# Optimization experiments

Measured on AMD Instinct MI355X. Metric: run time of the kernel, lower is better.

## Reference

```python
import jax, jax.numpy as jnp
import numpy as np

P = 22536   # priors
B = 32      # batch
M = 16      # objects per image (fixed for jit)
C = 81      # classes incl. background
THRESHOLD = 0.5
ALPHA_REG = 1.0   # config.reg_weights
FL_ALPHA = 0.25
FL_GAMMA = 2.0
EPS = 1e-7


def cxcy_to_xy(c):
    return jnp.concatenate([c[..., :2] - c[..., 2:] / 2, c[..., :2] + c[..., 2:] / 2], -1)


def gcxgcy_to_cxcy(g, p):
    return jnp.concatenate([g[..., :2] * p[..., 2:] / 10 + p[..., :2],
                            jnp.exp(g[..., 2:] / 5) * p[..., 2:]], -1)


def iou_xy(a, b):
    # a: (M,4) xyxy, b: (P,4) xyxy -> (M,P)
    lt = jnp.maximum(a[:, None, :2], b[None, :, :2])
    rb = jnp.minimum(a[:, None, 2:], b[None, :, 2:])
    inter = jnp.prod(jnp.clip(rb - lt, 0.0), -1)
    area_a = jnp.prod(a[:, 2:] - a[:, :2], -1)
    area_b = jnp.prod(b[:, 2:] - b[:, :2], -1)
    return inter / (area_a[:, None] + area_b[None, :] - inter)


def diou_loss(p, g):
    # elementwise DIoU loss, p/g: (..., 4) xyxy -> (...)
    lt = jnp.maximum(p[..., :2], g[..., :2])
    rb = jnp.minimum(p[..., 2:], g[..., 2:])
    inter = jnp.prod(jnp.clip(rb - lt, 0.0), -1)
    ap = jnp.prod(p[..., 2:] - p[..., :2], -1)
    ag = jnp.prod(g[..., 2:] - g[..., :2], -1)
    iou = inter / (ap + ag - inter + EPS)
    cp = (p[..., :2] + p[..., 2:]) / 2
    cg = (g[..., :2] + g[..., 2:]) / 2
    d2 = jnp.sum((cp - cg) ** 2, -1)
    elt = jnp.minimum(p[..., :2], g[..., :2])
    erb = jnp.maximum(p[..., 2:], g[..., 2:])
    c2 = jnp.sum((erb - elt) ** 2, -1) + EPS
    return 1.0 - iou + d2 / c2


def match_image(boxes_i, labels_i, priors_xy):
    # boxes_i: (M,4), labels_i: (M,), priors_xy: (P,4)
    overlap = iou_xy(boxes_i, priors_xy)                 # (M,P)
    ofp = overlap.max(0)                                  # overlap_for_each_prior (P,)
    obj = jnp.argmax(overlap, 0)                          # object_for_each_prior (P,)
    pfo = jnp.argmax(overlap, 1)                          # prior_for_each_object (M,)
    obj = obj.at[pfo].set(jnp.arange(M))
    ofp = ofp.at[pfo].set(1.0)
    lab = labels_i[obj]                                   # (P,)
    lab_neg = jnp.where(ofp < THRESHOLD - 0.1, -1, lab)
    lab = jnp.where(ofp < THRESHOLD, 0, lab)
    true_locs = boxes_i[obj]                              # (P,4)
    return lab, lab_neg, true_locs


def setup_inputs() -> dict:
    key = jax.random.key(0)
    k1, k2, k3, k4, k5, k6, k7 = jax.random.split(key, 7)
    pcxy = jax.random.uniform(k1, (P, 2), minval=0.05, maxval=0.95)
    pwh = jax.random.uniform(k2, (P, 2), minval=0.02, maxval=0.3)
    priors_cxcy = jnp.concatenate([pcxy, pwh], -1)
    ctr = jax.random.uniform(k3, (B, M, 2), minval=0.2, maxval=0.8)
    wh = jax.random.uniform(k4, (B, M, 2), minval=0.05, maxval=0.3)
    boxes = jnp.concatenate([ctr - wh / 2, ctr + wh / 2], -1)
    labels = jax.random.randint(k5, (B, M), 1, C).astype(jnp.int32)
    predicted_locs = jax.random.normal(k6, (B, P, 4), dtype=jnp.float32)
    predicted_scores = jax.random.normal(k7, (B, P, C), dtype=jnp.float32)
    return {"predicted_locs": predicted_locs, "predicted_scores": predicted_scores,
            "boxes": boxes, "labels": labels, "priors_cxcy": priors_cxcy}


def reference(predicted_locs, predicted_scores, boxes, labels, priors_cxcy):
    priors_xy = cxcy_to_xy(priors_cxcy)
    lab, lab_neg, true_locs = jax.vmap(match_image, in_axes=(0, 0, None))(boxes, labels, priors_xy)
    decoded = cxcy_to_xy(gcxgcy_to_cxcy(predicted_locs, priors_cxcy))   # (B,P,4)
    pos = lab > 0
    neg = lab_neg == -1
    # DIoU localization loss, mean over positive priors
    loc = diou_loss(decoded, true_locs)                                 # (B,P)
    npos = jnp.maximum(pos.sum(), 1)
    loc_loss = jnp.sum(loc * pos) / npos
    # focal classification loss over union of positive and hard-negative priors
    logp = jax.nn.log_softmax(predicted_scores, -1)                     # (B,P,C)
    lp_t = jnp.take_along_axis(logp, lab[..., None], -1)[..., 0]        # (B,P)
    pt = jnp.exp(lp_t)
    fl = FL_ALPHA * (1.0 - pt) ** FL_GAMMA * (-lp_t)
    m = pos | neg
    conf_loss = jnp.sum(fl * m) / jnp.maximum(m.sum(), 1)
    return conf_loss + ALPHA_REG * loc_loss
```

## Files before the change

### kernel.cpp

```cpp
#include <hip/hip_runtime.h>
#include <math.h>

#define PN 22536
#define BN 32
#define MN 16
#define CN 81
#define NMB ((PN + 255) / 256)
#define NCB 2048

__global__ __launch_bounds__(256)
void pfo_kernel(const float* __restrict__ boxes,
                const float* __restrict__ priors,
                unsigned long long* __restrict__ pfo_key)
{
    const int b = blockIdx.y;
    const int p = blockIdx.x * 256 + threadIdx.x;

    __shared__ float4 sbox[MN];
    __shared__ float  sarea[MN];
    __shared__ unsigned long long skey[MN];
    if (threadIdx.x < MN) {
        float4 bx = reinterpret_cast<const float4*>(boxes)[b * MN + threadIdx.x];
        sbox[threadIdx.x]  = bx;
        sarea[threadIdx.x] = (bx.z - bx.x) * (bx.w - bx.y);
        skey[threadIdx.x]  = 0ull;
    }
    __syncthreads();

    float x0 = 0.f, y0 = 0.f, x1 = 0.f, y1 = 0.f, ab = 0.f;
    const bool valid = (p < PN);
    if (valid) {
        float4 pc = reinterpret_cast<const float4*>(priors)[p];
        float hw = pc.z / 2.0f, hh = pc.w / 2.0f;
        x0 = pc.x - hw; y0 = pc.y - hh;
        x1 = pc.x + hw; y1 = pc.y + hh;
        ab = (x1 - x0) * (y1 - y0);
    }

    const int lane = threadIdx.x & 63;
    #pragma unroll
    for (int m = 0; m < MN; ++m) {
        unsigned long long key = 0ull;
        if (valid) {
            float4 bx = sbox[m];
            float lx = fmaxf(bx.x, x0), ly = fmaxf(bx.y, y0);
            float rx = fminf(bx.z, x1), ry = fminf(bx.w, y1);
            float inter = fmaxf(rx - lx, 0.0f) * fmaxf(ry - ly, 0.0f);
            float iou = inter / (sarea[m] + ab - inter);
            key = ((unsigned long long)__float_as_uint(iou) << 32) |
                  (unsigned long long)(~(unsigned int)p);
        }
        #pragma unroll
        for (int off = 32; off >= 1; off >>= 1) {
            unsigned long long o = __shfl_down(key, (unsigned)off, 64);
            if (o > key) key = o;
        }
        if (lane == 0) atomicMax(&skey[m], key);
    }
    __syncthreads();
    if (threadIdx.x < MN)
        atomicMax(&pfo_key[b * MN + threadIdx.x], skey[threadIdx.x]);
}

__global__ __launch_bounds__(256)
void match_kernel(const float* __restrict__ boxes,
                  const int*   __restrict__ labels,
                  const float* __restrict__ priors,
                  const float* __restrict__ plocs,
                  const unsigned long long* __restrict__ pfo_key,
                  unsigned char* __restrict__ labbyte,
                  float4* __restrict__ mpart)
{
    const int b = blockIdx.y;
    const int p = blockIdx.x * 256 + threadIdx.x;

    __shared__ float4 sbox[MN];
    __shared__ float  sarea[MN];
    __shared__ int    slab[MN];
    __shared__ int    spfo[MN];
    __shared__ float  sred[4][3];

    if (threadIdx.x < MN) {
        float4 bx = reinterpret_cast<const float4*>(boxes)[b * MN + threadIdx.x];
        sbox[threadIdx.x]  = bx;
        sarea[threadIdx.x] = (bx.z - bx.x) * (bx.w - bx.y);
        slab[threadIdx.x]  = labels[b * MN + threadIdx.x];
        spfo[threadIdx.x]  = (int)(~(unsigned int)(pfo_key[b * MN + threadIdx.x] &
                                                   0xFFFFFFFFull));
    }
    __syncthreads();

    float loc = 0.f, mc = 0.f, psc = 0.f;
    if (p < PN) {
        float4 pc = reinterpret_cast<const float4*>(priors)[p];
        float hw = pc.z / 2.0f, hh = pc.w / 2.0f;
        float qx0 = pc.x - hw, qy0 = pc.y - hh;
        float qx1 = pc.x + hw, qy1 = pc.y + hh;
        float ab  = (qx1 - qx0) * (qy1 - qy0);

        float best = -1.0f;
        int bestm = 0;
        #pragma unroll
        for (int m = 0; m < MN; ++m) {
            float4 bx = sbox[m];
            float lx = fmaxf(bx.x, qx0), ly = fmaxf(bx.y, qy0);
            float rx = fminf(bx.z, qx1), ry = fminf(bx.w, qy1);
            float inter = fmaxf(rx - lx, 0.0f) * fmaxf(ry - ly, 0.0f);
            float iou = inter / (sarea[m] + ab - inter);
            if (iou > best) { best = iou; bestm = m; }
        }
        #pragma unroll
        for (int m = 0; m < MN; ++m)
            if (spfo[m] == p) { bestm = m; best = 1.0f; }

        bool pos = best >= 0.5f;
        bool neg = best < 0.4f;
        labbyte[(size_t)b * PN + p] =
            pos ? (unsigned char)slab[bestm] : (neg ? (unsigned char)0
                                                    : (unsigned char)255);
        if (pos || neg) mc = 1.0f;

        if (pos) {
            float4 g = reinterpret_cast<const float4*>(plocs)[(size_t)b * PN + p];
            float cx = g.x * pc.z / 10.0f + pc.x;
            float cy = g.y * pc.w / 10.0f + pc.y;
            float ww = expf(g.z / 5.0f) * pc.z;
            float hh2 = expf(g.w / 5.0f) * pc.w;
            float px0 = cx - ww / 2.0f, py0 = cy - hh2 / 2.0f;
            float px1 = cx + ww / 2.0f, py1 = cy + hh2 / 2.0f;

            float4 gb = sbox[bestm];
            float lx = fmaxf(px0, gb.x), ly = fmaxf(py0, gb.y);
            float rx = fminf(px1, gb.z), ry = fminf(py1, gb.w);
            float inter = fmaxf(rx - lx, 0.f) * fmaxf(ry - ly, 0.f);
            float apx = (px1 - px0) * (py1 - py0);
            float agx = (gb.z - gb.x) * (gb.w - gb.y);
            float iou = inter / (apx + agx - inter + 1e-7f);
            float cpx = (px0 + px1) / 2.0f, cpy = (py0 + py1) / 2.0f;
            float cgx = (gb.x + gb.z) / 2.0f, cgy = (gb.y + gb.w) / 2.0f;
            float dx = cpx - cgx, dy = cpy - cgy;
            float d2 = dx * dx + dy * dy;
            float ex0 = fminf(px0, gb.x), ey0 = fminf(py0, gb.y);
            float ex1 = fmaxf(px1, gb.z), ey1 = fmaxf(py1, gb.w);
            float ew = ex1 - ex0, eh = ey1 - ey0;
            float c2 = ew * ew + eh * eh + 1e-7f;
            loc = 1.0f - iou + d2 / c2;
            psc = 1.0f;
        }
    }

    #pragma unroll
    for (int off = 32; off >= 1; off >>= 1) {
        loc += __shfl_down(loc, (unsigned)off, 64);
        mc  += __shfl_down(mc,  (unsigned)off, 64);
        psc += __shfl_down(psc, (unsigned)off, 64);
    }
    const int lane = threadIdx.x & 63;
    const int w = threadIdx.x >> 6;
    if (lane == 0) { sred[w][0] = loc; sred[w][1] = mc; sred[w][2] = psc; }
    __syncthreads();
    if (threadIdx.x == 0) {
        float a = 0.f, bsum = 0.f, c = 0.f;
        #pragma unroll
        for (int i = 0; i < 4; ++i) {
            a += sred[i][0]; bsum += sred[i][1]; c += sred[i][2];
        }
        mpart[b * NMB + blockIdx.x] = make_float4(a, c, bsum, 0.f);
    }
}

__global__ __launch_bounds__(256)
void conf_kernel(const float* __restrict__ scores,
                 const unsigned char* __restrict__ labbyte,
                 float* __restrict__ cpart)
{
    const int lane = threadIdx.x & 63;
    const int j    = lane & 15;
    const int g    = (lane >> 4);
    const int wave_g = (blockIdx.x * 256 + threadIdx.x) >> 6;
    const int stride = NCB * 16;
    const int R = BN * PN;

    float conf = 0.f;

    for (int row = wave_g * 4 + g; row < R; row += stride) {
        int lb = labbyte[row];
        if (lb == 255) continue;

        const float* srow = scores + (size_t)row * CN;
        float v0 = srow[j];
        float v1 = srow[j + 16];
        float v2 = srow[j + 32];
        float v3 = srow[j + 48];
        float v4 = srow[j + 64];
        float v5 = (j == 0) ? srow[80] : -INFINITY;

        float mx = fmaxf(fmaxf(fmaxf(v0, v1), fmaxf(v2, v3)), fmaxf(v4, v5));
        #pragma unroll
        for (int off = 1; off < 16; off <<= 1)
            mx = fmaxf(mx, __shfl_xor(mx, off, 64));

        float es = expf(v0 - mx) + expf(v1 - mx) + expf(v2 - mx) +
                   expf(v3 - mx) + expf(v4 - mx) + expf(v5 - mx);
        #pragma unroll
        for (int off = 1; off < 16; off <<= 1)
            es += __shfl_xor(es, off, 64);

        int hi = lb >> 4, lo = lb & 15;
        float sel = v0;
        sel = (hi == 1) ? v1 : sel;
        sel = (hi == 2) ? v2 : sel;
        sel = (hi == 3) ? v3 : sel;
        sel = (hi == 4) ? v4 : sel;
        sel = (hi == 5) ? v5 : sel;
        float tv = __shfl(sel, (lane & 48) | lo, 64);

        float lp = tv - mx - logf(es);
        float pt = expf(lp);
        float om = 1.0f - pt;
        if (j == 0) conf += 0.25f * om * om * (-lp);
    }

    #pragma unroll
    for (int off = 1; off < 64; off <<= 1)
        conf += __shfl_xor(conf, off, 64);

    __shared__ float sred[4];
    if (lane == 0) sred[threadIdx.x >> 6] = conf;
    __syncthreads();
    if (threadIdx.x == 0)
        cpart[blockIdx.x] = sred[0] + sred[1] + sred[2] + sred[3];
}

__global__ __launch_bounds__(256)
void reduce_kernel(const float4* __restrict__ mpart,
                   const float*  __restrict__ cpart,
                   float* __restrict__ out)
{
    const int NM = BN * NMB;
    float loc = 0.f, pcnt = 0.f, mcnt = 0.f, conf = 0.f;
    for (int i = threadIdx.x; i < NM; i += 256) {
        float4 v = mpart[i];
        loc += v.x; pcnt += v.y; mcnt += v.z;
    }
    for (int i = threadIdx.x; i < NCB; i += 256)
        conf += cpart[i];

    #pragma unroll
    for (int off = 1; off < 64; off <<= 1) {
        loc  += __shfl_xor(loc,  off, 64);
        pcnt += __shfl_xor(pcnt, off, 64);
        mcnt += __shfl_xor(mcnt, off, 64);
        conf += __shfl_xor(conf, off, 64);
    }
    __shared__ float s[4][4];
    int lane = threadIdx.x & 63, w = threadIdx.x >> 6;
    if (lane == 0) { s[w][0] = loc; s[w][1] = pcnt; s[w][2] = mcnt; s[w][3] = conf; }
    __syncthreads();
    if (threadIdx.x == 0) {
        float L = 0.f, Pc = 0.f, Mc = 0.f, Cf = 0.f;
        #pragma unroll
        for (int i = 0; i < 4; ++i) {
            L += s[i][0]; Pc += s[i][1]; Mc += s[i][2]; Cf += s[i][3];
        }
        out[0] = Cf / fmaxf(Mc, 1.0f) + L / fmaxf(Pc, 1.0f);
    }
}

extern "C" void kernel_launch(void* const* d_in, const int* in_sizes, int n_in,
                              void* d_out, int out_size, void* d_ws, size_t ws_size,
                              hipStream_t stream)
{
    const float* plocs  = (const float*)d_in[0];
    const float* scores = (const float*)d_in[1];
    const float* boxes  = (const float*)d_in[2];
    const int*   labels = (const int*)d_in[3];
    const float* priors = (const float*)d_in[4];
    float* out = (float*)d_out;

    char* ws = (char*)d_ws;
    unsigned long long* pfo_key = (unsigned long long*)ws;
    unsigned char* labbyte = (unsigned char*)(ws + 4096);
    float4* mpart = (float4*)(ws + 4096 + 721152);
    float*  cpart = (float*)(ws + 4096 + 721152 + BN * NMB * 16);

    hipMemsetAsync(pfo_key, 0, BN * MN * sizeof(unsigned long long), stream);

    dim3 gA(NMB, BN);
    pfo_kernel<<<gA, 256, 0, stream>>>(boxes, priors, pfo_key);
    match_kernel<<<gA, 256, 0, stream>>>(boxes, labels, priors, plocs,
                                         pfo_key, labbyte, mpart);
    conf_kernel<<<NCB, 256, 0, stream>>>(scores, labbyte, cpart);
    reduce_kernel<<<1, 256, 0, stream>>>(mpart, cpart, out);
}
```

Before: 379.5 us.

## Stage score rows in LDS with coalesced float4 loads for focal loss

Rewrites the classification-loss kernel so each block copies 128 contiguous score rows into shared memory with float4 loads, then two threads per row compute the softmax denominator. This replaces the old scheme, where 16 lanes read each row with strided scalar loads and used shuffle reductions. It also drops the max subtraction in log-softmax, which risks overflow for large logits. The grid grows to thousands of blocks using about 41 KB of LDS each, and every row is loaded even when its label marks it as ignored.

```diff
diff --git a/kernel.cpp b/kernel.cpp
--- a/kernel.cpp
+++ b/kernel.cpp
@@ -6,7 +6,8 @@
 #define MN 16
 #define CN 81
 #define NMB ((PN + 255) / 256)
-#define NCB 2048
+#define RPB 128
+#define NCB2 (BN * PN / RPB)
 
 __global__ __launch_bounds__(256)
 void pfo_kernel(const float* __restrict__ boxes,
@@ -174,59 +175,41 @@
                  const unsigned char* __restrict__ labbyte,
                  float* __restrict__ cpart)
 {
-    const int lane = threadIdx.x & 63;
-    const int j    = lane & 15;
-    const int g    = (lane >> 4);
-    const int wave_g = (blockIdx.x * 256 + threadIdx.x) >> 6;
-    const int stride = NCB * 16;
-    const int R = BN * PN;
+    __shared__ float ls[RPB * CN];
+    __shared__ float sred[4];
+
+    const float4* src4 = reinterpret_cast<const float4*>(scores) +
+                         (size_t)blockIdx.x * (RPB * CN / 4);
+    float4* ls4 = reinterpret_cast<float4*>(ls);
+    for (int i = threadIdx.x; i < RPB * CN / 4; i += 256)
+        ls4[i] = src4[i];
+    __syncthreads();
+
+    const int rl  = threadIdx.x >> 1;
+    const int h   = threadIdx.x & 1;
+    const int row = blockIdx.x * RPB + rl;
+    const int lb  = labbyte[row];
 
     float conf = 0.f;
-
-    for (int row = wave_g * 4 + g; row < R; row += stride) {
-        int lb = labbyte[row];
-        if (lb == 255) continue;
-
-        const float* srow = scores + (size_t)row * CN;
-        float v0 = srow[j];
-        float v1 = srow[j + 16];
-        float v2 = srow[j + 32];
-        float v3 = srow[j + 48];
-        float v4 = srow[j + 64];
-        float v5 = (j == 0) ? srow[80] : -INFINITY;
-
-        float mx = fmaxf(fmaxf(fmaxf(v0, v1), fmaxf(v2, v3)), fmaxf(v4, v5));
-        #pragma unroll
-        for (int off = 1; off < 16; off <<= 1)
-            mx = fmaxf(mx, __shfl_xor(mx, off, 64));
-
-        float es = expf(v0 - mx) + expf(v1 - mx) + expf(v2 - mx) +
-                   expf(v3 - mx) + expf(v4 - mx) + expf(v5 - mx);
-        #pragma unroll
-        for (int off = 1; off < 16; off <<= 1)
-            es += __shfl_xor(es, off, 64);
-
-        int hi = lb >> 4, lo = lb & 15;
-        float sel = v0;
-        sel = (hi == 1) ? v1 : sel;
-        sel = (hi == 2) ? v2 : sel;
-        sel = (hi == 3) ? v3 : sel;
-        sel = (hi == 4) ? v4 : sel;
-        sel = (hi == 5) ? v5 : sel;
-        float tv = __shfl(sel, (lane & 48) | lo, 64);
-
-        float lp = tv - mx - logf(es);
+    if (lb != 255) {
+        const float* rp = ls + rl * CN;
+        const int i0 = h ? 41 : 0;
+        const int i1 = h ? 81 : 41;
+        float es = 0.f;
+        for (int i = i0; i < i1; ++i)
+            es += expf(rp[i]);
+        es += __shfl_xor(es, 1, 64);
+        float tv = rp[lb];
+        float lp = tv - logf(es);
         float pt = expf(lp);
         float om = 1.0f - pt;
-        if (j == 0) conf += 0.25f * om * om * (-lp);
+        if (h == 0) conf = 0.25f * om * om * (-lp);
     }
 
     #pragma unroll
     for (int off = 1; off < 64; off <<= 1)
         conf += __shfl_xor(conf, off, 64);
-
-    __shared__ float sred[4];
-    if (lane == 0) sred[threadIdx.x >> 6] = conf;
+    if ((threadIdx.x & 63) == 0) sred[threadIdx.x >> 6] = conf;
     __syncthreads();
     if (threadIdx.x == 0)
         cpart[blockIdx.x] = sred[0] + sred[1] + sred[2] + sred[3];
@@ -243,7 +226,7 @@
         float4 v = mpart[i];
         loc += v.x; pcnt += v.y; mcnt += v.z;
     }
-    for (int i = threadIdx.x; i < NCB; i += 256)
+    for (int i = threadIdx.x; i < NCB2; i += 256)
         conf += cpart[i];
 
     #pragma unroll
@@ -290,6 +273,6 @@
     pfo_kernel<<<gA, 256, 0, stream>>>(boxes, priors, pfo_key);
     match_kernel<<<gA, 256, 0, stream>>>(boxes, labels, priors, plocs,
                                          pfo_key, labbyte, mpart);
-    conf_kernel<<<NCB, 256, 0, stream>>>(scores, labbyte, cpart);
+    conf_kernel<<<NCB2, 256, 0, stream>>>(scores, labbyte, cpart);
     reduce_kernel<<<1, 256, 0, stream>>>(mpart, cpart, out);
 }
```

Result: slower. 412.2 us (+8.6%).
